# Kernel tuning notes

Hardware: AMD Instinct MI355X
Metric: run time of the kernel (lower is better)

The kernel has to match this reference:

```python
import jax, jax.numpy as jnp
import numpy as np

B, C, H, W = 8, 192, 128, 128
CQK = C // 3  # 64


def setup_inputs() -> dict:
    key = jax.random.key(0)
    ks = jax.random.split(key, 8)
    s = 0.05
    return {
        "x": jax.random.normal(ks[0], (B, C, H, W), dtype=jnp.float32),
        "Wq": jax.random.normal(ks[1], (CQK, C), dtype=jnp.float32) * s,
        "bq": jax.random.normal(ks[2], (CQK,), dtype=jnp.float32) * s,
        "Wk": jax.random.normal(ks[3], (CQK, C), dtype=jnp.float32) * s,
        "bk": jax.random.normal(ks[4], (CQK,), dtype=jnp.float32) * s,
        "Wv": jax.random.normal(ks[5], (C, C), dtype=jnp.float32) * s,
        "bv": jax.random.normal(ks[6], (C,), dtype=jnp.float32) * s,
        "gamma": jnp.zeros((1,), dtype=jnp.float32),
    }


def _conv1x1(x, Wt, b):
    # x: [B,C,H,W], Wt: [Cout,Cin] -> [B,Cout,H,W]
    return jnp.einsum('bchw,oc->bohw', x, Wt) + b[None, :, None, None]


def reference(x, Wq, bq, Wk, bk, Wv, bv, gamma):
    Q = _conv1x1(x, Wq, bq)  # [B,CQK,H,W]
    K = _conv1x1(x, Wk, bk)  # [B,CQK,H,W]
    V = _conv1x1(x, Wv, bv)  # [B,C,H,W]

    # Column (vertical) attention logits: query at (h,w) attends to (h2,w)
    e_h = jnp.einsum('bchw,bcgw->bhwg', Q, K)  # [B,H,W,H]
    # mask diagonal h==h2 with -inf (as in MaskAttention)
    diag = jnp.where(jnp.eye(H, dtype=bool), -jnp.inf, 0.0).astype(x.dtype)
    e_h = e_h + diag[:, None, :]  # broadcast over B and W

    # Row (horizontal) attention logits: query at (h,w) attends to (h,w2)
    e_w = jnp.einsum('bchw,bchv->bhwv', Q, K)  # [B,H,W,W]

    # joint softmax over concatenated H+W axis
    att = jax.nn.softmax(jnp.concatenate([e_h, e_w], axis=3), axis=3)
    att_h = att[:, :, :, :H]      # [B,H,W,H]
    att_w = att[:, :, :, H:]      # [B,H,W,W]

    out_h = jnp.einsum('bhwg,bcgw->bchw', att_h, V)
    out_w = jnp.einsum('bhwv,bchv->bchw', att_w, V)
    return gamma * (out_h + out_w) + x
```

## Files before the change

kernel.cpp:

```cpp
#include <hip/hip_runtime.h>
#include <math.h>


#define B_   8
#define C_   192
#define CQK_ 64
#define H_   128
#define W_   128
#define HW_  (H_*W_)

typedef unsigned short u16;
typedef __attribute__((ext_vector_type(8))) short    s16x8;
typedef __attribute__((ext_vector_type(4))) float    f32x4;
typedef __attribute__((ext_vector_type(2))) unsigned u32x2;
#define MFMA_BF16 __builtin_amdgcn_mfma_f32_16x16x32_bf16

__device__ __forceinline__ u16 f2b(float f) {
    unsigned u = __float_as_uint(f);
    return (u16)((u + 0x7fffu + ((u >> 16) & 1u)) >> 16);
}
__device__ __forceinline__ float b2f(u16 v) {
    return __uint_as_float(((unsigned)v) << 16);
}
__device__ __forceinline__ void gll16(const u16* gsrc, unsigned lds_byte) {
    asm volatile("s_mov_b32 m0, %1\n\t"
                 "global_load_lds_dwordx4 %0, off"
                 :: "v"(gsrc), "s"(lds_byte) : "memory");
}

__global__ __launch_bounds__(256) void kwcast(
    const float* __restrict__ Wq, const float* __restrict__ bq,
    const float* __restrict__ Wk, const float* __restrict__ bk,
    const float* __restrict__ Wv, const float* __restrict__ bv,
    u16* __restrict__ Wb, float* __restrict__ Bb)
{
    const int o = blockIdx.x;
    const float *row, *bias; int oo;
    if (o < 64)        { row = Wq; bias = bq; oo = o;       }
    else if (o < 128)  { row = Wk; bias = bk; oo = o - 64;  }
    else               { row = Wv; bias = bv; oo = o - 128; }
    const int t = threadIdx.x;
    if (t < C_) {
        const int p = t >> 6, cc = t & 63;
        Wb[p*20480 + o*64 + (((cc >> 3) ^ (o & 7)) << 3) + (cc & 7)]
            = f2b(row[oo*C_ + t]);
    }
    if (t == C_) Bb[o] = bias[oo];
}

__global__ __launch_bounds__(256) void kxt(
    const float* __restrict__ x, u16* __restrict__ xT)
{
    __shared__ u16 T[24576];
    const int h = blockIdx.x, b = blockIdx.y;
    const float* xb = x + (size_t)b*C_*HW_ + h*W_;
    const int t = threadIdx.x;
    #pragma unroll
    for (int i = 0; i < 24; ++i) {
        const int ridx = i*256 + t;
        const int c = ridx >> 5, wq = (ridx & 31) << 2;
        const f32x4 v = *(const f32x4*)(const void*)(xb + (size_t)c*HW_ + wq);
        u32x2 pk;
        pk.x = (unsigned)f2b(v[0]) | ((unsigned)f2b(v[1]) << 16);
        pk.y = (unsigned)f2b(v[2]) | ((unsigned)f2b(v[3]) << 16);
        *(u32x2*)(void*)&T[c*128 + (((wq >> 3) ^ ((c >> 3) & 15)) << 3) + (wq & 7)] = pk;
    }
    __syncthreads();
    u16* dst = xT + (size_t)(b*H_ + h)*24576;
    #pragma unroll
    for (int i = 0; i < 12; ++i) {
        const int oidx = i*256 + t;
        const int p = oidx >> 10, w = (oidx >> 3) & 127, cp = oidx & 7;
        s16x8 pk;
        #pragma unroll
        for (int e = 0; e < 8; ++e) {
            const int c = p*64 + ((cp ^ (w & 7)) << 3) + e;
            pk[e] = (short)T[c*128 + ((((w >> 3)) ^ ((c >> 3) & 15)) << 3) + (w & 7)];
        }
        *(s16x8*)(void*)(dst + p*8192 + w*64 + cp*8) = pk;
    }
}

__global__ __launch_bounds__(256, 2) void kprojM(
    const u16* __restrict__ xT,
    const u16* __restrict__ Wb, const float* __restrict__ Bb,
    u16* __restrict__ Qc, u16* __restrict__ Kc, u16* __restrict__ Vn)
{
    __shared__ u16 lds[36864];
    u16* ldsW = lds + 16384;
    u16* ldsV = lds + 8192;
    const int h = blockIdx.x, b = blockIdx.y;
    const int t = threadIdx.x, lane = t & 63, wid = t >> 6;
    const int l15 = lane & 15, q = lane >> 4;

    f32x4 acc[8][5];
    #pragma unroll
    for (int ct = 0; ct < 5; ++ct) {
        const float bv = Bb[(ct*4 + wid)*16 + l15];
        #pragma unroll
        for (int r = 0; r < 8; ++r) acc[r][ct] = (f32x4){bv, bv, bv, bv};
    }

    const u16* xTb = xT + (size_t)(b*H_ + h)*24576;
    const unsigned wofs = __builtin_amdgcn_readfirstlane(32768u + (unsigned)wid*1024u);
    const unsigned aofs = __builtin_amdgcn_readfirstlane((unsigned)wid*1024u);

#define STAGE_W(p) do {                                                   \
    const u16* g = Wb + (p)*20480 + wid*512 + lane*8;                     \
    _Pragma("unroll")                                                     \
    for (int i = 0; i < 10; ++i) gll16(g + i*2048, wofs + i*4096); } while(0)
#define STAGE_A(p, ab) do {                                               \
    const u16* g = xTb + (p)*8192 + wid*512 + lane*8;                     \
    _Pragma("unroll")                                                     \
    for (int i = 0; i < 4; ++i)                                           \
        gll16(g + i*2048, aofs + (ab)*16384u + i*4096); } while(0)
#define MFMA_PHASE(ab) do {                                               \
    const u16* bA = lds + (ab)*8192;                                      \
    __builtin_amdgcn_s_setprio(1);                                        \
    _Pragma("unroll")                                                     \
    for (int ks = 0; ks < 2; ++ks) {                                      \
        s16x8 bf[5];                                                      \
        _Pragma("unroll")                                                 \
        for (int ct = 0; ct < 5; ++ct) {                                  \
            const int o = (ct*4 + wid)*16 + l15;                          \
            bf[ct] = *(const s16x8*)(const void*)                         \
                     &ldsW[o*64 + (((ks*4 + q) ^ (o & 7)) << 3)];         \
        }                                                                 \
        _Pragma("unroll")                                                 \
        for (int r = 0; r < 8; ++r) {                                     \
            const int w = r*16 + l15;                                     \
            const s16x8 af = *(const s16x8*)(const void*)                 \
                     &bA[w*64 + (((ks*4 + q) ^ (w & 7)) << 3)];           \
            _Pragma("unroll")                                             \
            for (int ct = 0; ct < 5; ++ct)                                \
                acc[r][ct] = MFMA_BF16(af, bf[ct], acc[r][ct], 0, 0, 0);  \
        }                                                                 \
    }                                                                     \
    __builtin_amdgcn_s_setprio(0); } while(0)

    STAGE_W(0); STAGE_A(0, 0); STAGE_A(1, 1);
    asm volatile("s_waitcnt vmcnt(4)" ::: "memory");
    __builtin_amdgcn_s_barrier();
    MFMA_PHASE(0);
    asm volatile("s_waitcnt lgkmcnt(0)" ::: "memory");
    __builtin_amdgcn_s_barrier();
    STAGE_W(1); STAGE_A(2, 0);
    asm volatile("s_waitcnt vmcnt(4)" ::: "memory");
    __builtin_amdgcn_s_barrier();
    MFMA_PHASE(1);
    asm volatile("s_waitcnt lgkmcnt(0)" ::: "memory");
    __builtin_amdgcn_s_barrier();
    STAGE_W(2);
    asm volatile("s_waitcnt vmcnt(0)" ::: "memory");
    __builtin_amdgcn_s_barrier();
    MFMA_PHASE(0);
    asm volatile("s_waitcnt lgkmcnt(0)" ::: "memory");
    __builtin_amdgcn_s_barrier();

    {
        const int oc = wid*16 + l15;
        #pragma unroll
        for (int r = 0; r < 8; ++r)
            #pragma unroll
            for (int rg = 0; rg < 4; ++rg) {
                const int w = r*16 + q*4 + rg;
                const size_t base = ((size_t)(b*W_ + w)*H_ + h)*CQK_ + oc;
                Qc[base] = f2b(acc[r][0][rg]);
                Kc[base] = f2b(acc[r][1][rg]);
            }
    }
    #pragma unroll
    for (int ct = 2; ct < 5; ++ct) {
        const int c = (ct - 2)*64 + wid*16 + l15;
        #pragma unroll
        for (int r = 0; r < 8; ++r) {
            const int w0 = r*16 + q*4;
            u32x2 pk;
            pk.x = (unsigned)f2b(acc[r][ct][0]) | ((unsigned)f2b(acc[r][ct][1]) << 16);
            pk.y = (unsigned)f2b(acc[r][ct][2]) | ((unsigned)f2b(acc[r][ct][3]) << 16);
            *(u32x2*)(void*)&ldsV[c*128 + (((w0 >> 3) ^ (c & 7)) << 3) + (w0 & 7)] = pk;
        }
    }
    asm volatile("s_waitcnt lgkmcnt(0)" ::: "memory");
    __builtin_amdgcn_s_barrier();
    #pragma unroll
    for (int i = 0; i < 12; ++i) {
        const int idx = i*256 + t;
        const int c = idx >> 4, j = idx & 15;
        const s16x8 v = *(const s16x8*)(const void*)&ldsV[c*128 + j*8];
        *(s16x8*)(void*)&Vn[(size_t)(b*C_ + c)*HW_ + h*W_ + ((j ^ (c & 7)) << 3)] = v;
    }
#undef STAGE_W
#undef STAGE_A
#undef MFMA_PHASE
}

__global__ __launch_bounds__(256) void ktrv(
    const u16* __restrict__ Vn, u16* __restrict__ Vc)
{
    __shared__ u16 T[128*128];
    const int c = blockIdx.x, b = blockIdx.y;
    const u16* src = Vn + (size_t)(b*C_ + c)*HW_;
    u16*       dst = Vc + (size_t)(b*C_ + c)*HW_;
    const int t = threadIdx.x;
    for (int idx = t; idx < 128*16; idx += 256) {
        const int hh = idx >> 4, o = idx & 15;
        s16x8 v = *(const s16x8*)(void*)(src + hh*128 + o*8);
        *(s16x8*)(void*)(T + hh*128 + ((o ^ (hh & 7)) << 3)) = v;
    }
    __syncthreads();
    const int w = t & 127, half = t >> 7;
    for (int seg = 0; seg < 8; ++seg) {
        const int h0 = half*64 + seg*8;
        s16x8 pk;
        #pragma unroll
        for (int k = 0; k < 8; ++k) {
            const int hh = h0 + k;
            const int chunk = (w >> 3) ^ (hh & 7);
            pk[k] = (short)T[hh*128 + (chunk << 3) + (w & 7)];
        }
        *(s16x8*)(void*)(dst + w*128 + h0) = pk;
    }
}

__global__ __launch_bounds__(512, 6) void kC(
    const u16* __restrict__ Qc, const u16* __restrict__ Kc,
    const u16* __restrict__ Vc,
    u16* __restrict__ O2, float* __restrict__ Mh, float* __restrict__ Sh)
{
    extern __shared__ char smem[];
    char* ldsK = smem;
    char* ldsP = smem;
    char* ldsV = smem + 32768;
    const int w = blockIdx.x, b = blockIdx.y;
    const int t = threadIdx.x, lane = t & 63, wid = t >> 6;
    const int l15 = lane & 15, q = lane >> 4;
    const int arow = (wid << 4) + l15;

    const u16* qrow = Qc + ((size_t)(b*W_ + w)*H_ + arow)*CQK_;
    s16x8 qf0 = *(const s16x8*)(const void*)(qrow + q*8);
    s16x8 qf1 = *(const s16x8*)(const void*)(qrow + (4 + q)*8);
    s16x8 vh[2];
    #pragma unroll
    for (int i = 0; i < 2; ++i) {
        const int idx = i*512 + t;
        const int c = 64 + (idx >> 4), o = idx & 15;
        vh[i] = *(const s16x8*)(const void*)
                (Vc + ((size_t)(b*C_ + c)*W_ + w)*H_ + o*8);
    }
    {
        const u16* ksrc = Kc + (size_t)(b*W_ + w)*H_*CQK_;
        for (int idx = t; idx < 1024; idx += 512) {
            const int r = idx >> 3, o = idx & 7;
            *(s16x8*)(ldsK + r*128 + ((o ^ (r & 7)) << 4)) =
                *(const s16x8*)(const void*)(ksrc + idx*8);
        }
    }
    for (int idx = t; idx < 1024; idx += 512) {
        const int lc = idx >> 4, o = idx & 15;
        *(s16x8*)(ldsV + lc*256 + ((o ^ (lc & 7)) << 4)) =
            *(const s16x8*)(const void*)
            (Vc + ((size_t)(b*C_ + lc)*W_ + w)*H_ + o*8);
    }
    __syncthreads();

    f32x4 accS[8];
    #pragma unroll
    for (int i = 0; i < 8; ++i) accS[i] = (f32x4){0.f,0.f,0.f,0.f};
    #pragma unroll
    for (int ks = 0; ks < 2; ++ks) {
        const int ch = ks*4 + q;
        const s16x8 af = ks ? qf1 : qf0;
        #pragma unroll
        for (int gt = 0; gt < 8; ++gt) {
            const int br = (gt << 4) + l15;
            s16x8 bf = *(const s16x8*)(ldsK + br*128 + ((ch ^ (br & 7)) << 4));
            accS[gt] = MFMA_BF16(af, bf, accS[gt], 0, 0, 0);
        }
    }
    __syncthreads();

    #pragma unroll
    for (int r = 0; r < 4; ++r) {
        const int hh = (wid << 4) + (q << 2) + r;
        #pragma unroll
        for (int gt = 0; gt < 8; ++gt)
            if ((gt << 4) + l15 == hh) accS[gt][r] = -3.0e38f;
        float m = -3.0e38f;
        #pragma unroll
        for (int gt = 0; gt < 8; ++gt) m = fmaxf(m, accS[gt][r]);
        m = fmaxf(m, __shfl_xor(m, 1)); m = fmaxf(m, __shfl_xor(m, 2));
        m = fmaxf(m, __shfl_xor(m, 4)); m = fmaxf(m, __shfl_xor(m, 8));
        float s = 0.f;
        #pragma unroll
        for (int gt = 0; gt < 8; ++gt) {
            const float e = __expf(accS[gt][r] - m);
            s += e;
            const int g = (gt << 4) + l15;
            *(u16*)(ldsP + hh*256 + (((g >> 3) ^ (hh & 7)) << 4) + (g & 7)*2)
                = f2b(e);
        }
        s += __shfl_xor(s, 1); s += __shfl_xor(s, 2);
        s += __shfl_xor(s, 4); s += __shfl_xor(s, 8);
        if (l15 == 0) {
            Mh[(b*W_ + w)*H_ + hh] = m;
            Sh[(b*W_ + w)*H_ + hh] = s;
        }
    }

#define KC_PV(accv) do {                                                  \
    _Pragma("unroll")                                                     \
    for (int ks = 0; ks < 4; ++ks) {                                      \
        const int ch = ks*4 + q;                                          \
        s16x8 afp = *(const s16x8*)(ldsP + arow*256 + ((ch ^ (arow & 7)) << 4)); \
        _Pragma("unroll")                                                 \
        for (int ct = 0; ct < 4; ++ct) {                                  \
            const int vr = (ct << 4) + l15;                               \
            s16x8 bfv = *(const s16x8*)(ldsV + vr*256 + ((ch ^ (vr & 7)) << 4)); \
            accv[ct] = MFMA_BF16(afp, bfv, accv[ct], 0, 0, 0);            \
        }                                                                 \
    } } while(0)
#define KC_O2W(accv, cb) do {                                             \
    _Pragma("unroll")                                                     \
    for (int ct = 0; ct < 4; ++ct) {                                      \
        const int c = (cb) + (ct << 4) + l15;                             \
        _Pragma("unroll")                                                 \
        for (int r = 0; r < 4; ++r) {                                     \
            const int hh = (wid << 4) + (q << 2) + r;                     \
            O2[((size_t)(b*H_ + hh)*W_ + w)*C_ + c] = f2b(accv[ct][r]);   \
        }                                                                 \
    } } while(0)

    f32x4 accO[4];
    #pragma unroll
    for (int i = 0; i < 4; ++i) accO[i] = (f32x4){0.f,0.f,0.f,0.f};
    KC_PV(accO);
    __syncthreads();
    #pragma unroll
    for (int i = 0; i < 2; ++i) {
        const int idx = i*512 + t;
        const int lc = idx >> 4, o = idx & 15;
        *(s16x8*)(ldsV + lc*256 + ((o ^ (lc & 7)) << 4)) = vh[i];
    }
    #pragma unroll
    for (int i = 0; i < 2; ++i) {
        const int idx = i*512 + t;
        const int c = 128 + (idx >> 4), o = idx & 15;
        vh[i] = *(const s16x8*)(const void*)
                (Vc + ((size_t)(b*C_ + c)*W_ + w)*H_ + o*8);
    }
    __syncthreads();
    KC_O2W(accO, 0);
    #pragma unroll
    for (int i = 0; i < 4; ++i) accO[i] = (f32x4){0.f,0.f,0.f,0.f};
    KC_PV(accO);
    __syncthreads();
    #pragma unroll
    for (int i = 0; i < 2; ++i) {
        const int idx = i*512 + t;
        const int lc = idx >> 4, o = idx & 15;
        *(s16x8*)(ldsV + lc*256 + ((o ^ (lc & 7)) << 4)) = vh[i];
    }
    __syncthreads();
    KC_O2W(accO, 64);
    #pragma unroll
    for (int i = 0; i < 4; ++i) accO[i] = (f32x4){0.f,0.f,0.f,0.f};
    KC_PV(accO);
    KC_O2W(accO, 128);
#undef KC_PV
#undef KC_O2W
}

__global__ __launch_bounds__(512, 6) void kR(
    const u16* __restrict__ Qc, const u16* __restrict__ Kc,
    const u16* __restrict__ Vn, const u16* __restrict__ O2,
    const float* __restrict__ Mh, const float* __restrict__ Sh,
    const float* __restrict__ x, const float* __restrict__ gamma,
    float* __restrict__ out)
{
    extern __shared__ char smem[];
    char*  ldsK  = smem;
    char*  ldsP  = smem;
    char*  ldsV  = smem + 32768;
    float* sScw  = (float*)(smem + 49152);
    float* sSch  = (float*)(smem + 49664);
    const int h = blockIdx.x, b = blockIdx.y;
    const int t = threadIdx.x, lane = t & 63, wid = t >> 6;
    const int l15 = lane & 15, q = lane >> 4;
    const int arow = (wid << 4) + l15;
    const int wbase = (wid << 4) + (q << 2);
    const float gam = gamma[0];

    const u16* qrow = Qc + ((size_t)(b*W_ + arow)*H_ + h)*CQK_;
    s16x8 qf0 = *(const s16x8*)(const void*)(qrow + q*8);
    s16x8 qf1 = *(const s16x8*)(const void*)(qrow + (4 + q)*8);
    s16x8 vh[2];
    #pragma unroll
    for (int i = 0; i < 2; ++i) {
        const int idx = i*512 + t;
        const int c = 64 + (idx >> 4), o = idx & 15;
        vh[i] = *(const s16x8*)(const void*)
                (Vn + (size_t)(b*C_ + c)*HW_ + h*W_ + o*8);
    }
    for (int idx = t; idx < 1024; idx += 512) {
        const int r = idx >> 3, o = idx & 7;
        *(s16x8*)(ldsK + r*128 + ((o ^ (r & 7)) << 4)) =
            *(const s16x8*)(const void*)
            (Kc + ((size_t)(b*W_ + r)*H_ + h)*CQK_ + o*8);
    }
    for (int idx = t; idx < 1024; idx += 512) {
        const int lc = idx >> 4, o = idx & 15;
        *(s16x8*)(ldsV + lc*256 + ((o ^ (lc & 7)) << 4)) =
            *(const s16x8*)(const void*)
            (Vn + (size_t)(b*C_ + lc)*HW_ + h*W_ + o*8);
    }
    __syncthreads();

    f32x4 accS[8];
    #pragma unroll
    for (int i = 0; i < 8; ++i) accS[i] = (f32x4){0.f,0.f,0.f,0.f};
    #pragma unroll
    for (int ks = 0; ks < 2; ++ks) {
        const int ch = ks*4 + q;
        const s16x8 af = ks ? qf1 : qf0;
        #pragma unroll
        for (int vt = 0; vt < 8; ++vt) {
            const int br = (vt << 4) + l15;
            s16x8 bf = *(const s16x8*)(ldsK + br*128 + ((ch ^ (br & 7)) << 4));
            accS[vt] = MFMA_BF16(af, bf, accS[vt], 0, 0, 0);
        }
    }
    __syncthreads();

    #pragma unroll
    for (int r = 0; r < 4; ++r) {
        const int ww = (wid << 4) + (q << 2) + r;
        float m = -3.0e38f;
        #pragma unroll
        for (int vt = 0; vt < 8; ++vt) m = fmaxf(m, accS[vt][r]);
        m = fmaxf(m, __shfl_xor(m, 1)); m = fmaxf(m, __shfl_xor(m, 2));
        m = fmaxf(m, __shfl_xor(m, 4)); m = fmaxf(m, __shfl_xor(m, 8));
        float s = 0.f;
        #pragma unroll
        for (int vt = 0; vt < 8; ++vt) {
            const float e = __expf(accS[vt][r] - m);
            s += e;
            const int v = (vt << 4) + l15;
            *(u16*)(ldsP + ww*256 + (((v >> 3) ^ (ww & 7)) << 4) + (v & 7)*2)
                = f2b(e);
        }
        s += __shfl_xor(s, 1); s += __shfl_xor(s, 2);
        s += __shfl_xor(s, 4); s += __shfl_xor(s, 8);
        if (l15 == 0) {
            const float mh  = Mh[(b*W_ + ww)*H_ + h];
            const float shv = Sh[(b*W_ + ww)*H_ + h];
            const float M = fmaxf(mh, m);
            const float S = shv*__expf(mh - M) + s*__expf(m - M);
            sScw[ww] = __expf(m - M) / S;
            sSch[ww] = __expf(mh - M) / S;
        }
    }
    float scw[4], sch[4];
    #pragma unroll
    for (int r = 0; r < 4; ++r) { scw[r] = sScw[wbase + r]; sch[r] = sSch[wbase + r]; }

    const u16* o2p = O2 + (size_t)(b*H_ + h)*W_*C_;

#define KR_PV(accv) do {                                                  \
    _Pragma("unroll")                                                     \
    for (int ks = 0; ks < 4; ++ks) {                                      \
        const int ch = ks*4 + q;                                          \
        s16x8 afp = *(const s16x8*)(ldsP + arow*256 + ((ch ^ (arow & 7)) << 4)); \
        _Pragma("unroll")                                                 \
        for (int ct = 0; ct < 4; ++ct) {                                  \
            const int vr = (ct << 4) + l15;                               \
            s16x8 bfv = *(const s16x8*)(ldsV + vr*256 + ((ch ^ (vr & 7)) << 4)); \
            accv[ct] = MFMA_BF16(afp, bfv, accv[ct], 0, 0, 0);            \
        }                                                                 \
    } } while(0)
#define KR_EPI(k, accv) do {                                              \
    _Pragma("unroll")                                                     \
    for (int ct = 0; ct < 4; ++ct) {                                      \
        const int c = (k)*64 + (ct << 4) + l15;                           \
        const size_t ga = (size_t)(b*C_ + c)*HW_ + h*W_ + wbase;          \
        const f32x4 xv = *(const f32x4*)(const void*)(x + ga);            \
        f32x4 res;                                                        \
        _Pragma("unroll")                                                 \
        for (int r = 0; r < 4; ++r) {                                     \
            const float o2 = b2f(o2p[(size_t)(wbase + r)*C_ + c]);        \
            res[r] = gam*(accv[ct][r]*scw[r] + o2*sch[r]) + xv[r];        \
        }                                                                 \
        *(f32x4*)(void*)(out + ga) = res;                                 \
    } } while(0)

    f32x4 accO[4];
    #pragma unroll
    for (int i = 0; i < 4; ++i) accO[i] = (f32x4){0.f,0.f,0.f,0.f};
    KR_PV(accO);
    __syncthreads();
    #pragma unroll
    for (int i = 0; i < 2; ++i) {
        const int idx = i*512 + t;
        const int lc = idx >> 4, o = idx & 15;
        *(s16x8*)(ldsV + lc*256 + ((o ^ (lc & 7)) << 4)) = vh[i];
    }
    #pragma unroll
    for (int i = 0; i < 2; ++i) {
        const int idx = i*512 + t;
        const int c = 128 + (idx >> 4), o = idx & 15;
        vh[i] = *(const s16x8*)(const void*)
                (Vn + (size_t)(b*C_ + c)*HW_ + h*W_ + o*8);
    }
    KR_EPI(0, accO);
    __syncthreads();
    #pragma unroll
    for (int i = 0; i < 4; ++i) accO[i] = (f32x4){0.f,0.f,0.f,0.f};
    KR_PV(accO);
    __syncthreads();
    #pragma unroll
    for (int i = 0; i < 2; ++i) {
        const int idx = i*512 + t;
        const int lc = idx >> 4, o = idx & 15;
        *(s16x8*)(ldsV + lc*256 + ((o ^ (lc & 7)) << 4)) = vh[i];
    }
    KR_EPI(1, accO);
    __syncthreads();
    #pragma unroll
    for (int i = 0; i < 4; ++i) accO[i] = (f32x4){0.f,0.f,0.f,0.f};
    KR_PV(accO);
    KR_EPI(2, accO);
#undef KR_PV
#undef KR_EPI
}

extern "C" void kernel_launch(void* const* d_in, const int* in_sizes, int n_in,
                              void* d_out, int out_size, void* d_ws, size_t ws_size,
                              hipStream_t stream)
{
    const float* x  = (const float*)d_in[0];
    const float* Wq = (const float*)d_in[1];
    const float* bq = (const float*)d_in[2];
    const float* Wk = (const float*)d_in[3];
    const float* bk = (const float*)d_in[4];
    const float* Wv = (const float*)d_in[5];
    const float* bv = (const float*)d_in[6];
    const float* gm = (const float*)d_in[7];
    float* out = (float*)d_out;

    u16* Qc = (u16*)d_ws;
    u16* Kc = Qc + 8388608;
    u16* Vn = Kc + 8388608;
    u16* Vc = Vn + 25165824;
    u16* O2 = Vc + 25165824;
    u16* xT = O2;
    float* Mh = (float*)(O2 + 25165824);
    float* Sh = Mh + 131072;
    u16*  Wb = (u16*)(Sh + 131072);
    float* Bb = (float*)(Wb + 61440);

    hipLaunchKernelGGL(kwcast, dim3(320), dim3(256), 0, stream,
                       Wq, bq, Wk, bk, Wv, bv, Wb, Bb);
    hipLaunchKernelGGL(kxt, dim3(H_, B_), dim3(256), 0, stream, x, xT);
    hipLaunchKernelGGL(kprojM, dim3(H_, B_), dim3(256), 0, stream,
                       xT, Wb, Bb, Qc, Kc, Vn);
    hipLaunchKernelGGL(ktrv, dim3(C_, B_), dim3(256), 0, stream, Vn, Vc);
    hipLaunchKernelGGL(kC, dim3(W_, B_), dim3(512), 49152, stream,
                       Qc, Kc, Vc, O2, Mh, Sh);
    hipLaunchKernelGGL(kR, dim3(H_, B_), dim3(512), 50176, stream,
                       Qc, Kc, Vn, O2, Mh, Sh, x, gm, out);
}
```

Baseline: 197.9 us.

## Fuse x transpose/bf16 cast into projection kernel and relax attention launch bounds

```diff
diff --git a/kernel.cpp b/kernel.cpp
--- a/kernel.cpp
+++ b/kernel.cpp
@@ -48,50 +48,19 @@
     if (t == C_) Bb[o] = bias[oo];
 }
 
-__global__ __launch_bounds__(256) void kxt(
-    const float* __restrict__ x, u16* __restrict__ xT)
-{
-    __shared__ u16 T[24576];
-    const int h = blockIdx.x, b = blockIdx.y;
-    const float* xb = x + (size_t)b*C_*HW_ + h*W_;
-    const int t = threadIdx.x;
-    #pragma unroll
-    for (int i = 0; i < 24; ++i) {
-        const int ridx = i*256 + t;
-        const int c = ridx >> 5, wq = (ridx & 31) << 2;
-        const f32x4 v = *(const f32x4*)(const void*)(xb + (size_t)c*HW_ + wq);
-        u32x2 pk;
-        pk.x = (unsigned)f2b(v[0]) | ((unsigned)f2b(v[1]) << 16);
-        pk.y = (unsigned)f2b(v[2]) | ((unsigned)f2b(v[3]) << 16);
-        *(u32x2*)(void*)&T[c*128 + (((wq >> 3) ^ ((c >> 3) & 15)) << 3) + (wq & 7)] = pk;
-    }
-    __syncthreads();
-    u16* dst = xT + (size_t)(b*H_ + h)*24576;
-    #pragma unroll
-    for (int i = 0; i < 12; ++i) {
-        const int oidx = i*256 + t;
-        const int p = oidx >> 10, w = (oidx >> 3) & 127, cp = oidx & 7;
-        s16x8 pk;
-        #pragma unroll
-        for (int e = 0; e < 8; ++e) {
-            const int c = p*64 + ((cp ^ (w & 7)) << 3) + e;
-            pk[e] = (short)T[c*128 + ((((w >> 3)) ^ ((c >> 3) & 15)) << 3) + (w & 7)];
-        }
-        *(s16x8*)(void*)(dst + p*8192 + w*64 + cp*8) = pk;
-    }
-}
-
 __global__ __launch_bounds__(256, 2) void kprojM(
-    const u16* __restrict__ xT,
+    const float* __restrict__ x,
     const u16* __restrict__ Wb, const float* __restrict__ Bb,
     u16* __restrict__ Qc, u16* __restrict__ Kc, u16* __restrict__ Vn)
 {
-    __shared__ u16 lds[36864];
-    u16* ldsW = lds + 16384;
-    u16* ldsV = lds + 8192;
+    __shared__ u16 lds[28672];
+    u16* ldsA = lds;
+    u16* ldsW = lds + 8192;
     const int h = blockIdx.x, b = blockIdx.y;
     const int t = threadIdx.x, lane = t & 63, wid = t >> 6;
     const int l15 = lane & 15, q = lane >> 4;
+    const float* xb = x + (size_t)b*C_*HW_ + h*W_;
+    const int wql = t & 127, cpair = (t >> 7) << 1;
 
     f32x4 acc[8][5];
     #pragma unroll
@@ -101,21 +70,29 @@
         for (int r = 0; r < 8; ++r) acc[r][ct] = (f32x4){bv, bv, bv, bv};
     }
 
-    const u16* xTb = xT + (size_t)(b*H_ + h)*24576;
-    const unsigned wofs = __builtin_amdgcn_readfirstlane(32768u + (unsigned)wid*1024u);
-    const unsigned aofs = __builtin_amdgcn_readfirstlane((unsigned)wid*1024u);
+    const unsigned wofs = __builtin_amdgcn_readfirstlane(16384u + (unsigned)wid*1024u);
+    float va0[16], va1[16];
 
 #define STAGE_W(p) do {                                                   \
     const u16* g = Wb + (p)*20480 + wid*512 + lane*8;                     \
     _Pragma("unroll")                                                     \
     for (int i = 0; i < 10; ++i) gll16(g + i*2048, wofs + i*4096); } while(0)
-#define STAGE_A(p, ab) do {                                               \
-    const u16* g = xTb + (p)*8192 + wid*512 + lane*8;                     \
-    _Pragma("unroll")                                                     \
-    for (int i = 0; i < 4; ++i)                                           \
-        gll16(g + i*2048, aofs + (ab)*16384u + i*4096); } while(0)
-#define MFMA_PHASE(ab) do {                                               \
-    const u16* bA = lds + (ab)*8192;                                      \
+#define LOAD_A(p) do {                                                    \
+    _Pragma("unroll")                                                     \
+    for (int i = 0; i < 16; ++i) {                                        \
+        const int c = i*4 + cpair;                                        \
+        va0[i] = xb[(size_t)((p)*64 + c    )*HW_ + wql];                  \
+        va1[i] = xb[(size_t)((p)*64 + c + 1)*HW_ + wql];                  \
+    } } while(0)
+#define WRITE_A() do {                                                    \
+    _Pragma("unroll")                                                     \
+    for (int i = 0; i < 16; ++i) {                                        \
+        const int c = i*4 + cpair;                                        \
+        const unsigned pk = (unsigned)f2b(va0[i]) | ((unsigned)f2b(va1[i]) << 16); \
+        *(unsigned*)(void*)&ldsA[wql*64 + (((c >> 3) ^ (wql & 7)) << 3)   \
+                                 + (c & 7)] = pk;                         \
+    } } while(0)
+#define MFMA_PHASE() do {                                                 \
     __builtin_amdgcn_s_setprio(1);                                        \
     _Pragma("unroll")                                                     \
     for (int ks = 0; ks < 2; ++ks) {                                      \
@@ -130,7 +107,7 @@
         for (int r = 0; r < 8; ++r) {                                     \
             const int w = r*16 + l15;                                     \
             const s16x8 af = *(const s16x8*)(const void*)                 \
-                     &bA[w*64 + (((ks*4 + q) ^ (w & 7)) << 3)];           \
+                     &ldsA[w*64 + (((ks*4 + q) ^ (w & 7)) << 3)];         \
             _Pragma("unroll")                                             \
             for (int ct = 0; ct < 5; ++ct)                                \
                 acc[r][ct] = MFMA_BF16(af, bf[ct], acc[r][ct], 0, 0, 0);  \
@@ -138,22 +115,28 @@
     }                                                                     \
     __builtin_amdgcn_s_setprio(0); } while(0)
 
-    STAGE_W(0); STAGE_A(0, 0); STAGE_A(1, 1);
-    asm volatile("s_waitcnt vmcnt(4)" ::: "memory");
-    __builtin_amdgcn_s_barrier();
-    MFMA_PHASE(0);
+    LOAD_A(0);
+    STAGE_W(0);
+    WRITE_A();
+    LOAD_A(1);
+    asm volatile("s_waitcnt lgkmcnt(0) vmcnt(32)" ::: "memory");
+    __builtin_amdgcn_s_barrier();
+    MFMA_PHASE();
     asm volatile("s_waitcnt lgkmcnt(0)" ::: "memory");
     __builtin_amdgcn_s_barrier();
-    STAGE_W(1); STAGE_A(2, 0);
-    asm volatile("s_waitcnt vmcnt(4)" ::: "memory");
-    __builtin_amdgcn_s_barrier();
-    MFMA_PHASE(1);
+    STAGE_W(1);
+    WRITE_A();
+    LOAD_A(2);
+    asm volatile("s_waitcnt lgkmcnt(0) vmcnt(32)" ::: "memory");
+    __builtin_amdgcn_s_barrier();
+    MFMA_PHASE();
     asm volatile("s_waitcnt lgkmcnt(0)" ::: "memory");
     __builtin_amdgcn_s_barrier();
     STAGE_W(2);
-    asm volatile("s_waitcnt vmcnt(0)" ::: "memory");
-    __builtin_amdgcn_s_barrier();
-    MFMA_PHASE(0);
+    WRITE_A();
+    asm volatile("s_waitcnt lgkmcnt(0) vmcnt(0)" ::: "memory");
+    __builtin_amdgcn_s_barrier();
+    MFMA_PHASE();
     asm volatile("s_waitcnt lgkmcnt(0)" ::: "memory");
     __builtin_amdgcn_s_barrier();
 
@@ -169,6 +152,7 @@
                 Kc[base] = f2b(acc[r][1][rg]);
             }
     }
+    u16* ldsVe = lds;
     #pragma unroll
     for (int ct = 2; ct < 5; ++ct) {
         const int c = (ct - 2)*64 + wid*16 + l15;
@@ -178,7 +162,7 @@
             u32x2 pk;
             pk.x = (unsigned)f2b(acc[r][ct][0]) | ((unsigned)f2b(acc[r][ct][1]) << 16);
             pk.y = (unsigned)f2b(acc[r][ct][2]) | ((unsigned)f2b(acc[r][ct][3]) << 16);
-            *(u32x2*)(void*)&ldsV[c*128 + (((w0 >> 3) ^ (c & 7)) << 3) + (w0 & 7)] = pk;
+            *(u32x2*)(void*)&ldsVe[c*128 + (((w0 >> 3) ^ (c & 7)) << 3) + (w0 & 7)] = pk;
         }
     }
     asm volatile("s_waitcnt lgkmcnt(0)" ::: "memory");
@@ -187,11 +171,12 @@
     for (int i = 0; i < 12; ++i) {
         const int idx = i*256 + t;
         const int c = idx >> 4, j = idx & 15;
-        const s16x8 v = *(const s16x8*)(const void*)&ldsV[c*128 + j*8];
+        const s16x8 v = *(const s16x8*)(const void*)&ldsVe[c*128 + j*8];
         *(s16x8*)(void*)&Vn[(size_t)(b*C_ + c)*HW_ + h*W_ + ((j ^ (c & 7)) << 3)] = v;
     }
 #undef STAGE_W
-#undef STAGE_A
+#undef LOAD_A
+#undef WRITE_A
 #undef MFMA_PHASE
 }
 
@@ -223,7 +208,7 @@
     }
 }
 
-__global__ __launch_bounds__(512, 6) void kC(
+__global__ __launch_bounds__(512, 4) void kC(
     const u16* __restrict__ Qc, const u16* __restrict__ Kc,
     const u16* __restrict__ Vc,
     u16* __restrict__ O2, float* __restrict__ Mh, float* __restrict__ Sh)
@@ -371,7 +356,7 @@
 #undef KC_O2W
 }
 
-__global__ __launch_bounds__(512, 6) void kR(
+__global__ __launch_bounds__(512, 4) void kR(
     const u16* __restrict__ Qc, const u16* __restrict__ Kc,
     const u16* __restrict__ Vn, const u16* __restrict__ O2,
     const float* __restrict__ Mh, const float* __restrict__ Sh,
@@ -552,7 +537,6 @@
     u16* Vn = Kc + 8388608;
     u16* Vc = Vn + 25165824;
     u16* O2 = Vc + 25165824;
-    u16* xT = O2;
     float* Mh = (float*)(O2 + 25165824);
     float* Sh = Mh + 131072;
     u16*  Wb = (u16*)(Sh + 131072);
@@ -560,9 +544,8 @@
 
     hipLaunchKernelGGL(kwcast, dim3(320), dim3(256), 0, stream,
                        Wq, bq, Wk, bk, Wv, bv, Wb, Bb);
-    hipLaunchKernelGGL(kxt, dim3(H_, B_), dim3(256), 0, stream, x, xT);
     hipLaunchKernelGGL(kprojM, dim3(H_, B_), dim3(256), 0, stream,
-                       xT, Wb, Bb, Qc, Kc, Vn);
+                       x, Wb, Bb, Qc, Kc, Vn);
     hipLaunchKernelGGL(ktrv, dim3(C_, B_), dim3(256), 0, stream, Vn, Vc);
     hipLaunchKernelGGL(kC, dim3(W_, B_), dim3(512), 49152, stream,
                        Qc, Kc, Vc, O2, Mh, Sh);
```

Result: faster. 189.5 us (-4.3%).
